# Optimization experiments

Hardware: AMD Instinct MI355X
Metric: run time of the kernel (lower is better)

Reference implementation:

```python
import math
import jax, jax.numpy as jnp
import numpy as np

H_HEADS = 8
K_MAX = 64
MIN_WINDOW = 1.0
SHARPNESS = 5.0


def rmsnorm(x, w, eps=1e-6):
    x32 = x.astype(jnp.float32)
    var = jnp.mean(x32 * x32, axis=-1, keepdims=True)
    return (w * (x32 * jax.lax.rsqrt(var + eps))).astype(x.dtype)


def setup_inputs() -> dict:
    key = jax.random.key(0)
    ks = jax.random.split(key, 12)
    B, L, C = 1, 4096, 256
    H, K = H_HEADS, K_MAX
    s = 0.02
    return {
        "x": jax.random.normal(ks[0], (B, L, C), jnp.float32),
        "window_w": jax.random.normal(ks[1], (C, H), jnp.float32) * s,
        "window_b": jnp.zeros((H,), jnp.float32),
        "window_gamma": jnp.ones((H,), jnp.float32),
        "offset_w": jax.random.normal(ks[2], (C, H), jnp.float32) * s,
        "offset_b": jnp.zeros((H,), jnp.float32),
        "offset_gamma": jnp.ones((H,), jnp.float32),
        "kernel_w": jax.random.normal(ks[3], (C, H * K), jnp.float32) * s,
        "kernel_b": jnp.zeros((H * K,), jnp.float32),
        "kernel_gamma": jnp.ones((H * K,), jnp.float32),
        "v_w": jax.random.normal(ks[4], (C, C), jnp.float32) * (1.0 / math.sqrt(C)),
        "v_b": jnp.zeros((C,), jnp.float32),
        "out_w": jax.random.normal(ks[5], (C, C), jnp.float32) * s,
    }


def reference(x, window_w, window_b, window_gamma, offset_w, offset_b, offset_gamma,
              kernel_w, kernel_b, kernel_gamma, v_w, v_b, out_w):
    B, L, C = x.shape
    H, K = H_HEADS, K_MAX
    D = C // H
    max_window = min(int(math.sqrt(L)), K)
    half = max_window // 2
    max_offset = int(math.sqrt(L))
    N = 2 * half + 1  # num_offsets

    # per-position learned window sizes, center offsets, kernel weights
    window_raw = jax.nn.sigmoid(rmsnorm(x @ window_w + window_b, window_gamma))
    window_sizes = MIN_WINDOW + window_raw * (max_window - MIN_WINDOW)      # [B,L,H]
    center_offsets = jnp.tanh(rmsnorm(x @ offset_w + offset_b, offset_gamma)) * max_offset  # [B,L,H]
    kernel_weights = jax.nn.silu(rmsnorm(x @ kernel_w + kernel_b, kernel_gamma)).reshape(B, L, H, K)
    v = (x @ v_w + v_b).reshape(B, L, H, D)

    local = jnp.arange(-half, half + 1, dtype=x.dtype)                      # [N]
    positions = jnp.arange(L, dtype=x.dtype).reshape(1, L, 1, 1)
    neighbor = positions + center_offsets[..., None] + local.reshape(1, 1, 1, N)  # [B,L,H,N]
    valid = (neighbor >= 0) & (neighbor < L)
    nclamp = jnp.clip(neighbor, 0, L - 1)

    rel = jnp.abs(local).reshape(1, 1, 1, N) / (window_sizes[..., None] / 2 + 1e-6)
    window_mask = jax.nn.sigmoid(SHARPNESS * (1.0 - rel)) * valid.astype(x.dtype)

    # kernel interpolation by relative distance
    kidx = jnp.clip(rel, 0, 1) * (K - 1)
    i_fl = jnp.clip(kidx.astype(jnp.int32), 0, K - 2)                       # [B,L,H,N]
    i_ce = i_fl + 1
    w_ce = kidx - i_fl.astype(x.dtype)
    k_fl = jnp.take_along_axis(kernel_weights, i_fl, axis=-1)
    k_ce = jnp.take_along_axis(kernel_weights, i_ce, axis=-1)
    kernel_interp = k_fl * (1.0 - w_ce) + k_ce * w_ce

    attn = kernel_interp * window_mask
    attn = attn / (jnp.sum(attn, axis=-1, keepdims=True) + 1e-6)            # [B,L,H,N]

    # bilinear gather of values at fractional neighbor positions
    p_fl = jnp.clip(jnp.floor(nclamp).astype(jnp.int32), 0, L - 1)
    p_ce = jnp.clip(p_fl + 1, 0, L - 1)
    frac = nclamp - p_fl.astype(x.dtype)                                    # [B,L,H,N]

    v_bh = v.transpose(0, 2, 1, 3)                                          # [B,H,L,D]
    idx_f = p_fl.transpose(0, 2, 1, 3).reshape(B, H, L * N)
    idx_c = p_ce.transpose(0, 2, 1, 3).reshape(B, H, L * N)
    v_fl = jnp.take_along_axis(v_bh, idx_f[..., None], axis=2).reshape(B, H, L, N, D)
    v_ce = jnp.take_along_axis(v_bh, idx_c[..., None], axis=2).reshape(B, H, L, N, D)
    frac_bh = frac.transpose(0, 2, 1, 3)[..., None]                         # [B,H,L,N,1]
    v_nb = v_fl * (1.0 - frac_bh) + v_ce * frac_bh                          # [B,H,L,N,D]

    attn_bh = attn.transpose(0, 2, 1, 3)                                    # [B,H,L,N]
    out = jnp.einsum('bhln,bhlnd->bhld', attn_bh, v_nb)                     # [B,H,L,D]
    out = out.transpose(0, 2, 1, 3).reshape(B, L, C)
    return jax.nn.silu(out @ out_w)
```

## Files before the change

### kernel.cpp

```cpp
#include <hip/hip_runtime.h>
#include <math.h>

#define L_SEQ 4096
#define C_DIM 256
#define H_HEADS 8
#define K_MAX 64
#define D_HEAD 32
#define HALF_W 32
#define N_OFF 65
#define HK 512

__device__ __forceinline__ float sigmoidf_(float x) { return 1.0f / (1.0f + expf(-x)); }

__global__ void proj_gemm(const float* __restrict__ A, const float* __restrict__ kw_w,
                          const float* __restrict__ vw, const float* __restrict__ kb,
                          const float* __restrict__ vb,
                          float* __restrict__ kwbuf, float* __restrict__ vbuf) {
    __shared__ float As[16][132];
    __shared__ float Bs[16][68];

    const int tid = threadIdx.x;
    const int tx = tid & 15;
    const int ty = tid >> 4;
    const int l0 = blockIdx.y * 128;
    const int n0 = blockIdx.x * 64;

    const int ar0 = tid >> 2;
    const int ac0 = (tid & 3) * 4;
    const int ar1 = ar0 + 64;
    const int bk = tid >> 4;
    const int bn = (tid & 15) * 4;

    const float* Bsrc;
    int ldb, coff;
    if (n0 < 512) { Bsrc = kw_w; ldb = 512; coff = n0; }
    else          { Bsrc = vw;   ldb = 256; coff = n0 - 512; }

    float acc[8][4];
#pragma unroll
    for (int i = 0; i < 8; ++i)
#pragma unroll
        for (int jj = 0; jj < 4; ++jj) acc[i][jj] = 0.0f;

    float4 av0 = *(const float4*)&A[(l0 + ar0) * C_DIM + ac0];
    float4 av1 = *(const float4*)&A[(l0 + ar1) * C_DIM + ac0];
    float4 bv  = *(const float4*)&Bsrc[bk * ldb + coff + bn];

    for (int k0 = 0; k0 < C_DIM; k0 += 16) {
        __syncthreads();
        As[ac0 + 0][ar0] = av0.x;
        As[ac0 + 1][ar0] = av0.y;
        As[ac0 + 2][ar0] = av0.z;
        As[ac0 + 3][ar0] = av0.w;
        As[ac0 + 0][ar1] = av1.x;
        As[ac0 + 1][ar1] = av1.y;
        As[ac0 + 2][ar1] = av1.z;
        As[ac0 + 3][ar1] = av1.w;
        *(float4*)&Bs[bk][bn] = bv;
        __syncthreads();
        if (k0 + 16 < C_DIM) {
            av0 = *(const float4*)&A[(l0 + ar0) * C_DIM + (k0 + 16) + ac0];
            av1 = *(const float4*)&A[(l0 + ar1) * C_DIM + (k0 + 16) + ac0];
            bv  = *(const float4*)&Bsrc[(k0 + 16 + bk) * ldb + coff + bn];
        }
#pragma unroll
        for (int kk = 0; kk < 16; ++kk) {
            const float4 a4lo = *(const float4*)&As[kk][ty * 8];
            const float4 a4hi = *(const float4*)&As[kk][ty * 8 + 4];
            const float4 b4   = *(const float4*)&Bs[kk][tx * 4];
            const float ar[8] = {a4lo.x, a4lo.y, a4lo.z, a4lo.w,
                                 a4hi.x, a4hi.y, a4hi.z, a4hi.w};
            const float br[4] = {b4.x, b4.y, b4.z, b4.w};
#pragma unroll
            for (int i = 0; i < 8; ++i)
#pragma unroll
                for (int jj = 0; jj < 4; ++jj)
                    acc[i][jj] = fmaf(ar[i], br[jj], acc[i][jj]);
        }
    }

    const int g0 = n0 + tx * 4;
    float4 bz;
    float* dst;
    int stride, col;
    if (g0 < 512) { bz = *(const float4*)&kb[g0];       dst = kwbuf; stride = 512; col = g0; }
    else          { bz = *(const float4*)&vb[g0 - 512]; dst = vbuf;  stride = 256; col = g0 - 512; }
#pragma unroll
    for (int i = 0; i < 8; ++i) {
        const int row = l0 + ty * 8 + i;
        float4 o;
        o.x = acc[i][0] + bz.x;
        o.y = acc[i][1] + bz.y;
        o.z = acc[i][2] + bz.z;
        o.w = acc[i][3] + bz.w;
        *(float4*)&dst[row * stride + col] = o;
    }
}

__global__ void conv_fused(const float* __restrict__ x,
                           const float* __restrict__ ww, const float* __restrict__ wb,
                           const float* __restrict__ wg,
                           const float* __restrict__ ow, const float* __restrict__ ob,
                           const float* __restrict__ og,
                           const float* __restrict__ kg,
                           const float* __restrict__ kwraw, const float* __restrict__ v,
                           float* __restrict__ out) {
    const int l = blockIdx.x;
    const int tid = threadIdx.x;

    __shared__ float red[256];
    __shared__ float rs_s;
    __shared__ float kwrow[HK];
    __shared__ float wsz[H_HEADS], ofs[H_HEADS];
    __shared__ float4 tap[H_HEADS][N_OFF];
    __shared__ float2 warr[H_HEADS][N_OFF + 1];
    __shared__ float inv_denom[H_HEADS];
    __shared__ int okflag;

    if (tid == 0) okflag = 1;

    {
        const int j = tid;
        const float* row = kwraw + l * HK;
        const float z0 = row[j];
        const float z1 = row[j + 256];
        red[j] = z0 * z0 + z1 * z1;
        __syncthreads();
        for (int s = 128; s > 0; s >>= 1) {
            if (j < s) red[j] += red[j + s];
            __syncthreads();
        }
        if (j == 0) rs_s = rsqrtf(red[0] / (float)HK + 1e-6f);
        __syncthreads();
        const float rs = rs_s;
        const float n0v = kg[j] * z0 * rs;
        const float n1v = kg[j + 256] * z1 * rs;
        kwrow[j]       = n0v * sigmoidf_(n0v);
        kwrow[j + 256] = n1v * sigmoidf_(n1v);
    }

    if (tid < 64) {
        const int lane = tid;
        const float* xr = x + l * C_DIM;
        float accw[H_HEADS], acco[H_HEADS];
#pragma unroll
        for (int h = 0; h < H_HEADS; ++h) { accw[h] = 0.0f; acco[h] = 0.0f; }
#pragma unroll
        for (int i = 0; i < C_DIM / 64; ++i) {
            const int c = lane + i * 64;
            const float xv = xr[c];
            const float* wwc = ww + c * H_HEADS;
            const float* owc = ow + c * H_HEADS;
#pragma unroll
            for (int h = 0; h < H_HEADS; ++h) {
                accw[h] = fmaf(xv, wwc[h], accw[h]);
                acco[h] = fmaf(xv, owc[h], acco[h]);
            }
        }
#pragma unroll
        for (int off = 32; off > 0; off >>= 1) {
#pragma unroll
            for (int h = 0; h < H_HEADS; ++h) {
                accw[h] += __shfl_xor(accw[h], off);
                acco[h] += __shfl_xor(acco[h], off);
            }
        }
        if (lane < H_HEADS) {
            float zw[H_HEADS], zo[H_HEADS];
            float ssw = 0.0f, sso = 0.0f;
#pragma unroll
            for (int h = 0; h < H_HEADS; ++h) {
                zw[h] = accw[h] + wb[h];
                zo[h] = acco[h] + ob[h];
                ssw += zw[h] * zw[h];
                sso += zo[h] * zo[h];
            }
            const float rw = rsqrtf(ssw / (float)H_HEADS + 1e-6f);
            const float ro = rsqrtf(sso / (float)H_HEADS + 1e-6f);
            const float nw = wg[lane] * zw[lane] * rw;
            const float no = og[lane] * zo[lane] * ro;
            wsz[lane] = 1.0f + sigmoidf_(nw) * 63.0f;
            ofs[lane] = tanhf(no) * 64.0f;
        }
    }
    __syncthreads();

    for (int t = tid; t < H_HEADS * N_OFF; t += 256) {
        const int h = t / N_OFF;
        const int n = t - h * N_OFF;
        const float ws  = wsz[h];
        const float off = ofs[h];
        const float local = (float)(n - HALF_W);
        const float neighbor = (float)l + off + local;
        const bool valid = (neighbor >= 0.0f) && (neighbor < (float)L_SEQ);
        const float nc = fminf(fmaxf(neighbor, 0.0f), (float)(L_SEQ - 1));

        const float rel = fabsf(local) / (ws * 0.5f + 1e-6f);
        const float mask = sigmoidf_(5.0f * (1.0f - rel)) * (valid ? 1.0f : 0.0f);

        const float kidx = fminf(rel, 1.0f) * (float)(K_MAX - 1);
        int ifl = (int)kidx;
        ifl = min(ifl, K_MAX - 2);
        const float wce = kidx - (float)ifl;
        const float kf = kwrow[h * K_MAX + ifl];
        const float kc = kwrow[h * K_MAX + ifl + 1];
        const float attnv = (kf * (1.0f - wce) + kc * wce) * mask;

        int p = (int)floorf(nc);
        p = min(max(p, 0), L_SEQ - 1);
        const int pc = min(p + 1, L_SEQ - 1);
        const float fr = nc - (float)p;

        float4 tv;
        tv.x = attnv;
        tv.y = fr;
        tv.z = __int_as_float(p * C_DIM + h * D_HEAD);
        tv.w = __int_as_float(pc * C_DIM + h * D_HEAD);
        tap[h][n] = tv;
    }
    __syncthreads();

    for (int t = tid; t < H_HEADS * (N_OFF + 1); t += 256) {
        const int h = t / (N_OFF + 1);
        const int m = t - h * (N_OFF + 1);
        float w, rowf;
        if (m == 0) {
            const float4 cur = tap[h][0];
            w = cur.x * (1.0f - cur.y);
            rowf = cur.z;
        } else {
            const float4 prev = tap[h][m - 1];
            const float wc = prev.x * prev.y;
            if (m < N_OFF) {
                const float4 cur = tap[h][m];
                w = cur.x * (1.0f - cur.y) + wc;
                rowf = cur.z;
                if (wc != 0.0f && __float_as_int(prev.w) != __float_as_int(cur.z))
                    okflag = 0;
            } else {
                w = wc;
                rowf = prev.w;
            }
        }
        warr[h][m] = make_float2(w, rowf);
    }

    if (tid < H_HEADS) {
        float s = 0.0f;
        for (int n = 0; n < N_OFF; ++n) s += tap[tid][n].x;
        inv_denom[tid] = 1.0f / (s + 1e-6f);
    }
    __syncthreads();

    const int h = tid >> 5;
    const int d = tid & 31;
    float acc = 0.0f;
    if (okflag) {
#pragma unroll 6
        for (int m = 0; m < N_OFF + 1; ++m) {
            const float2 t2 = warr[h][m];
            acc = fmaf(t2.x, v[__float_as_int(t2.y) + d], acc);
        }
    } else {
#pragma unroll 5
        for (int n = 0; n < N_OFF; ++n) {
            const float4 t4 = tap[h][n];
            const int bf = __float_as_int(t4.z);
            const int bc = __float_as_int(t4.w);
            const float vf = v[bf + d];
            const float vc = v[bc + d];
            acc = fmaf(t4.x, fmaf(t4.y, vc - vf, vf), acc);
        }
    }
    out[l * C_DIM + h * D_HEAD + d] = acc * inv_denom[h];
}

__global__ void out_gemm(const float* __restrict__ A, const float* __restrict__ W,
                         float* __restrict__ out) {
    __shared__ float As[16][68];
    __shared__ float Bs[16][68];

    const int tid = threadIdx.x;
    const int tx = tid & 15;
    const int ty = tid >> 4;
    const int l0 = blockIdx.y * 64;
    const int n0 = blockIdx.x * 64;

    const int am = tid >> 2;
    const int ak = (tid & 3) * 4;
    const int bk = tid >> 4;
    const int bn = (tid & 15) * 4;

    float acc[4][4];
#pragma unroll
    for (int i = 0; i < 4; ++i)
#pragma unroll
        for (int jj = 0; jj < 4; ++jj) acc[i][jj] = 0.0f;

    float4 av = *(const float4*)&A[(l0 + am) * C_DIM + ak];
    float4 bv = *(const float4*)&W[bk * C_DIM + n0 + bn];

    for (int k0 = 0; k0 < C_DIM; k0 += 16) {
        __syncthreads();
        As[ak + 0][am] = av.x;
        As[ak + 1][am] = av.y;
        As[ak + 2][am] = av.z;
        As[ak + 3][am] = av.w;
        *(float4*)&Bs[bk][bn] = bv;
        __syncthreads();
        if (k0 + 16 < C_DIM) {
            av = *(const float4*)&A[(l0 + am) * C_DIM + (k0 + 16) + ak];
            bv = *(const float4*)&W[(k0 + 16 + bk) * C_DIM + n0 + bn];
        }
#pragma unroll
        for (int kk = 0; kk < 16; ++kk) {
            const float4 a4 = *(const float4*)&As[kk][ty * 4];
            const float4 b4 = *(const float4*)&Bs[kk][tx * 4];
            const float ar[4] = {a4.x, a4.y, a4.z, a4.w};
            const float br[4] = {b4.x, b4.y, b4.z, b4.w};
#pragma unroll
            for (int i = 0; i < 4; ++i)
#pragma unroll
                for (int jj = 0; jj < 4; ++jj)
                    acc[i][jj] = fmaf(ar[i], br[jj], acc[i][jj]);
        }
    }

    const int g0 = n0 + tx * 4;
#pragma unroll
    for (int i = 0; i < 4; ++i) {
        const int row = l0 + ty * 4 + i;
        float4 o;
        o.x = acc[i][0] * sigmoidf_(acc[i][0]);
        o.y = acc[i][1] * sigmoidf_(acc[i][1]);
        o.z = acc[i][2] * sigmoidf_(acc[i][2]);
        o.w = acc[i][3] * sigmoidf_(acc[i][3]);
        *(float4*)&out[row * C_DIM + g0] = o;
    }
}

extern "C" void kernel_launch(void* const* d_in, const int* in_sizes, int n_in,
                              void* d_out, int out_size, void* d_ws, size_t ws_size,
                              hipStream_t stream) {
    const float* x    = (const float*)d_in[0];
    const float* ww   = (const float*)d_in[1];
    const float* wb   = (const float*)d_in[2];
    const float* wg   = (const float*)d_in[3];
    const float* ow   = (const float*)d_in[4];
    const float* ob   = (const float*)d_in[5];
    const float* og   = (const float*)d_in[6];
    const float* kw_w = (const float*)d_in[7];
    const float* kb   = (const float*)d_in[8];
    const float* kg   = (const float*)d_in[9];
    const float* vw   = (const float*)d_in[10];
    const float* vb   = (const float*)d_in[11];
    const float* outw = (const float*)d_in[12];
    float* y = (float*)d_out;

    float* ws_f    = (float*)d_ws;
    float* kwbuf   = ws_f;
    float* vbuf    = kwbuf + L_SEQ * HK;
    float* convbuf = vbuf + L_SEQ * C_DIM;

    proj_gemm<<<dim3(12, L_SEQ / 128), 256, 0, stream>>>(x, kw_w, vw, kb, vb, kwbuf, vbuf);
    conv_fused<<<L_SEQ, 256, 0, stream>>>(x, ww, wb, wg, ow, ob, og, kg, kwbuf, vbuf, convbuf);
    out_gemm<<<dim3(C_DIM / 64, L_SEQ / 64), 256, 0, stream>>>(convbuf, outw, y);
}
```

Before: 148.0 us.

## Widen GEMM thread tile and double conv block threads with split tap loop

```diff
diff --git a/kernel.cpp b/kernel.cpp
--- a/kernel.cpp
+++ b/kernel.cpp
@@ -20,80 +20,88 @@
     __shared__ float Bs[16][68];
 
     const int tid = threadIdx.x;
-    const int tx = tid & 15;
-    const int ty = tid >> 4;
+    const int tx = tid & 7;
+    const int ty = tid >> 3;
     const int l0 = blockIdx.y * 128;
     const int n0 = blockIdx.x * 64;
 
-    const int ar0 = tid >> 2;
-    const int ac0 = (tid & 3) * 4;
-    const int ar1 = ar0 + 64;
-    const int bk = tid >> 4;
-    const int bn = (tid & 15) * 4;
+    const int arow = tid;
+    const int bk = tid >> 3;
+    const int bn = (tid & 7) * 8;
 
     const float* Bsrc;
     int ldb, coff;
     if (n0 < 512) { Bsrc = kw_w; ldb = 512; coff = n0; }
     else          { Bsrc = vw;   ldb = 256; coff = n0 - 512; }
 
-    float acc[8][4];
+    float acc[8][8];
 #pragma unroll
     for (int i = 0; i < 8; ++i)
 #pragma unroll
-        for (int jj = 0; jj < 4; ++jj) acc[i][jj] = 0.0f;
-
-    float4 av0 = *(const float4*)&A[(l0 + ar0) * C_DIM + ac0];
-    float4 av1 = *(const float4*)&A[(l0 + ar1) * C_DIM + ac0];
-    float4 bv  = *(const float4*)&Bsrc[bk * ldb + coff + bn];
+        for (int jj = 0; jj < 8; ++jj) acc[i][jj] = 0.0f;
+
+    const float* arow_p = A + (l0 + arow) * C_DIM;
+    float4 a0 = *(const float4*)&arow_p[0];
+    float4 a1 = *(const float4*)&arow_p[4];
+    float4 a2 = *(const float4*)&arow_p[8];
+    float4 a3 = *(const float4*)&arow_p[12];
+    float4 b0 = *(const float4*)&Bsrc[bk * ldb + coff + bn];
+    float4 b1 = *(const float4*)&Bsrc[bk * ldb + coff + bn + 4];
 
     for (int k0 = 0; k0 < C_DIM; k0 += 16) {
         __syncthreads();
-        As[ac0 + 0][ar0] = av0.x;
-        As[ac0 + 1][ar0] = av0.y;
-        As[ac0 + 2][ar0] = av0.z;
-        As[ac0 + 3][ar0] = av0.w;
-        As[ac0 + 0][ar1] = av1.x;
-        As[ac0 + 1][ar1] = av1.y;
-        As[ac0 + 2][ar1] = av1.z;
-        As[ac0 + 3][ar1] = av1.w;
-        *(float4*)&Bs[bk][bn] = bv;
+        As[0][arow]  = a0.x; As[1][arow]  = a0.y; As[2][arow]  = a0.z; As[3][arow]  = a0.w;
+        As[4][arow]  = a1.x; As[5][arow]  = a1.y; As[6][arow]  = a1.z; As[7][arow]  = a1.w;
+        As[8][arow]  = a2.x; As[9][arow]  = a2.y; As[10][arow] = a2.z; As[11][arow] = a2.w;
+        As[12][arow] = a3.x; As[13][arow] = a3.y; As[14][arow] = a3.z; As[15][arow] = a3.w;
+        *(float4*)&Bs[bk][bn]     = b0;
+        *(float4*)&Bs[bk][bn + 4] = b1;
         __syncthreads();
         if (k0 + 16 < C_DIM) {
-            av0 = *(const float4*)&A[(l0 + ar0) * C_DIM + (k0 + 16) + ac0];
-            av1 = *(const float4*)&A[(l0 + ar1) * C_DIM + (k0 + 16) + ac0];
-            bv  = *(const float4*)&Bsrc[(k0 + 16 + bk) * ldb + coff + bn];
+            a0 = *(const float4*)&arow_p[k0 + 16 + 0];
+            a1 = *(const float4*)&arow_p[k0 + 16 + 4];
+            a2 = *(const float4*)&arow_p[k0 + 16 + 8];
+            a3 = *(const float4*)&arow_p[k0 + 16 + 12];
+            b0 = *(const float4*)&Bsrc[(k0 + 16 + bk) * ldb + coff + bn];
+            b1 = *(const float4*)&Bsrc[(k0 + 16 + bk) * ldb + coff + bn + 4];
         }
 #pragma unroll
         for (int kk = 0; kk < 16; ++kk) {
-            const float4 a4lo = *(const float4*)&As[kk][ty * 8];
-            const float4 a4hi = *(const float4*)&As[kk][ty * 8 + 4];
-            const float4 b4   = *(const float4*)&Bs[kk][tx * 4];
-            const float ar[8] = {a4lo.x, a4lo.y, a4lo.z, a4lo.w,
-                                 a4hi.x, a4hi.y, a4hi.z, a4hi.w};
-            const float br[4] = {b4.x, b4.y, b4.z, b4.w};
+            const float4 alo = *(const float4*)&As[kk][ty * 8];
+            const float4 ahi = *(const float4*)&As[kk][ty * 8 + 4];
+            const float4 blo = *(const float4*)&Bs[kk][tx * 8];
+            const float4 bhi = *(const float4*)&Bs[kk][tx * 8 + 4];
+            const float ar[8] = {alo.x, alo.y, alo.z, alo.w, ahi.x, ahi.y, ahi.z, ahi.w};
+            const float br[8] = {blo.x, blo.y, blo.z, blo.w, bhi.x, bhi.y, bhi.z, bhi.w};
 #pragma unroll
             for (int i = 0; i < 8; ++i)
 #pragma unroll
-                for (int jj = 0; jj < 4; ++jj)
+                for (int jj = 0; jj < 8; ++jj)
                     acc[i][jj] = fmaf(ar[i], br[jj], acc[i][jj]);
         }
     }
 
-    const int g0 = n0 + tx * 4;
-    float4 bz;
+    const int g0 = n0 + tx * 8;
+    float4 bz0, bz1;
     float* dst;
     int stride, col;
-    if (g0 < 512) { bz = *(const float4*)&kb[g0];       dst = kwbuf; stride = 512; col = g0; }
-    else          { bz = *(const float4*)&vb[g0 - 512]; dst = vbuf;  stride = 256; col = g0 - 512; }
+    if (g0 < 512) {
+        bz0 = *(const float4*)&kb[g0]; bz1 = *(const float4*)&kb[g0 + 4];
+        dst = kwbuf; stride = 512; col = g0;
+    } else {
+        bz0 = *(const float4*)&vb[g0 - 512]; bz1 = *(const float4*)&vb[g0 - 508];
+        dst = vbuf; stride = 256; col = g0 - 512;
+    }
 #pragma unroll
     for (int i = 0; i < 8; ++i) {
         const int row = l0 + ty * 8 + i;
-        float4 o;
-        o.x = acc[i][0] + bz.x;
-        o.y = acc[i][1] + bz.y;
-        o.z = acc[i][2] + bz.z;
-        o.w = acc[i][3] + bz.w;
-        *(float4*)&dst[row * stride + col] = o;
+        float4 o0, o1;
+        o0.x = acc[i][0] + bz0.x; o0.y = acc[i][1] + bz0.y;
+        o0.z = acc[i][2] + bz0.z; o0.w = acc[i][3] + bz0.w;
+        o1.x = acc[i][4] + bz1.x; o1.y = acc[i][5] + bz1.y;
+        o1.z = acc[i][6] + bz1.z; o1.w = acc[i][7] + bz1.w;
+        *(float4*)&dst[row * stride + col]     = o0;
+        *(float4*)&dst[row * stride + col + 4] = o1;
     }
 }
 
@@ -117,30 +125,14 @@
     __shared__ float inv_denom[H_HEADS];
     __shared__ int okflag;
 
-    if (tid == 0) okflag = 1;
-
-    {
-        const int j = tid;
+    float z0 = 0.0f, z1 = 0.0f;
+    if (tid < 256) {
         const float* row = kwraw + l * HK;
-        const float z0 = row[j];
-        const float z1 = row[j + 256];
-        red[j] = z0 * z0 + z1 * z1;
-        __syncthreads();
-        for (int s = 128; s > 0; s >>= 1) {
-            if (j < s) red[j] += red[j + s];
-            __syncthreads();
-        }
-        if (j == 0) rs_s = rsqrtf(red[0] / (float)HK + 1e-6f);
-        __syncthreads();
-        const float rs = rs_s;
-        const float n0v = kg[j] * z0 * rs;
-        const float n1v = kg[j + 256] * z1 * rs;
-        kwrow[j]       = n0v * sigmoidf_(n0v);
-        kwrow[j + 256] = n1v * sigmoidf_(n1v);
-    }
-
-    if (tid < 64) {
-        const int lane = tid;
+        z0 = row[tid];
+        z1 = row[tid + 256];
+        red[tid] = z0 * z0 + z1 * z1;
+    } else if (tid < 320) {
+        const int lane = tid - 256;
         const float* xr = x + l * C_DIM;
         float accw[H_HEADS], acco[H_HEADS];
 #pragma unroll
@@ -183,9 +175,34 @@
             ofs[lane] = tanhf(no) * 64.0f;
         }
     }
-    __syncthreads();
-
-    for (int t = tid; t < H_HEADS * N_OFF; t += 256) {
+    if (tid == 0) okflag = 1;
+    __syncthreads();
+
+    if (tid < 128) red[tid] += red[tid + 128];
+    __syncthreads();
+    if (tid < 64) {
+        red[tid] += red[tid + 64];
+        if (tid < 32) red[tid] += red[tid + 32];
+        if (tid < 16) red[tid] += red[tid + 16];
+        if (tid < 8)  red[tid] += red[tid + 8];
+        if (tid < 4)  red[tid] += red[tid + 4];
+        if (tid < 2)  red[tid] += red[tid + 2];
+        if (tid < 1) {
+            red[0] += red[1];
+            rs_s = rsqrtf(red[0] / (float)HK + 1e-6f);
+        }
+    }
+    __syncthreads();
+    if (tid < 256) {
+        const float rs = rs_s;
+        const float n0v = kg[tid] * z0 * rs;
+        const float n1v = kg[tid + 256] * z1 * rs;
+        kwrow[tid]       = n0v * sigmoidf_(n0v);
+        kwrow[tid + 256] = n1v * sigmoidf_(n1v);
+    }
+    __syncthreads();
+
+    for (int t = tid; t < H_HEADS * N_OFF; t += 512) {
         const int h = t / N_OFF;
         const int n = t - h * N_OFF;
         const float ws  = wsz[h];
@@ -220,7 +237,7 @@
     }
     __syncthreads();
 
-    for (int t = tid; t < H_HEADS * (N_OFF + 1); t += 256) {
+    for (int t = tid; t < H_HEADS * (N_OFF + 1); t += 512) {
         const int h = t / (N_OFF + 1);
         const int m = t - h * (N_OFF + 1);
         float w, rowf;
@@ -252,27 +269,31 @@
     }
     __syncthreads();
 
-    const int h = tid >> 5;
-    const int d = tid & 31;
+    const int h = tid >> 6;
+    const int lane = tid & 63;
+    const int half = lane >> 5;
+    const int d = lane & 31;
     float acc = 0.0f;
     if (okflag) {
-#pragma unroll 6
-        for (int m = 0; m < N_OFF + 1; ++m) {
-            const float2 t2 = warr[h][m];
+#pragma unroll 3
+        for (int it = 0; it < (N_OFF + 1) / 2; ++it) {
+            const float2 t2 = warr[h][2 * it + half];
             acc = fmaf(t2.x, v[__float_as_int(t2.y) + d], acc);
         }
     } else {
-#pragma unroll 5
-        for (int n = 0; n < N_OFF; ++n) {
-            const float4 t4 = tap[h][n];
-            const int bf = __float_as_int(t4.z);
-            const int bc = __float_as_int(t4.w);
-            const float vf = v[bf + d];
-            const float vc = v[bc + d];
-            acc = fmaf(t4.x, fmaf(t4.y, vc - vf, vf), acc);
-        }
-    }
-    out[l * C_DIM + h * D_HEAD + d] = acc * inv_denom[h];
+#pragma unroll 3
+        for (int it = 0; it < 33; ++it) {
+            const int n = 2 * it + half;
+            if (n < N_OFF) {
+                const float4 t4 = tap[h][n];
+                const float vf = v[__float_as_int(t4.z) + d];
+                const float vc = v[__float_as_int(t4.w) + d];
+                acc = fmaf(t4.x, fmaf(t4.y, vc - vf, vf), acc);
+            }
+        }
+    }
+    acc += __shfl_xor(acc, 32);
+    if (half == 0) out[l * C_DIM + h * D_HEAD + d] = acc * inv_denom[h];
 }
 
 __global__ void out_gemm(const float* __restrict__ A, const float* __restrict__ W,
@@ -362,7 +383,7 @@
     float* vbuf    = kwbuf + L_SEQ * HK;
     float* convbuf = vbuf + L_SEQ * C_DIM;
 
-    proj_gemm<<<dim3(12, L_SEQ / 128), 256, 0, stream>>>(x, kw_w, vw, kb, vb, kwbuf, vbuf);
-    conv_fused<<<L_SEQ, 256, 0, stream>>>(x, ww, wb, wg, ow, ob, og, kg, kwbuf, vbuf, convbuf);
+    proj_gemm<<<dim3(12, L_SEQ / 128), 128, 0, stream>>>(x, kw_w, vw, kb, vb, kwbuf, vbuf);
+    conv_fused<<<L_SEQ, 512, 0, stream>>>(x, ww, wb, wg, ow, ob, og, kg, kwbuf, vbuf, convbuf);
     out_gemm<<<dim3(C_DIM / 64, L_SEQ / 64), 256, 0, stream>>>(convbuf, outw, y);
 }
```

New measurement: 221.5 us. 1.5x slower.
